# Performance work log

Hardware: AMD Instinct MI355X
Metric: run time of the kernel (lower is better)

## Reference

```python
import jax, jax.numpy as jnp
from jax import lax
import numpy as np

B, D, H, T = 64, 32, 512, 1024


def setup_inputs() -> dict:
    key = jax.random.key(0)
    ks = jax.random.split(key, 7)
    s = 1.0 / np.sqrt(H)
    return {
        "input_data": jax.random.normal(ks[0], (B, D, T), dtype=jnp.float32),
        "W_ih": jax.random.uniform(ks[1], (4 * H, D), jnp.float32, -s, s),
        "W_hh": jax.random.uniform(ks[2], (4 * H, H), jnp.float32, -s, s),
        "b_ih": jax.random.uniform(ks[3], (4 * H,), jnp.float32, -s, s),
        "b_hh": jax.random.uniform(ks[4], (4 * H,), jnp.float32, -s, s),
        "conv_w": jax.random.uniform(ks[5], (1, H, 1), jnp.float32, -s, s),
        "conv_b": jax.random.uniform(ks[6], (1,), jnp.float32, -s, s),
    }


def reference(input_data, W_ih, W_hh, b_ih, b_hh, conv_w, conv_b):
    # (B, D, T) -> (T, B, D), seq-first like torch nn.LSTM
    x = jnp.transpose(input_data, (2, 0, 1))
    # Precompute input-to-gate projections for all timesteps: (T, B, 4H)
    xproj = jnp.einsum('tbd,gd->tbg', x, W_ih) + b_ih + b_hh
    h0 = jnp.zeros((x.shape[1], H), x.dtype)
    c0 = jnp.zeros((x.shape[1], H), x.dtype)

    def step(carry, xp):
        h, c = carry
        gates = xp + h @ W_hh.T  # (B, 4H)
        i, f, g, o = jnp.split(gates, 4, axis=-1)  # torch gate order: i, f, g, o
        i = jax.nn.sigmoid(i)
        f = jax.nn.sigmoid(f)
        g = jnp.tanh(g)
        o = jax.nn.sigmoid(o)
        c_new = f * c + i * g
        h_new = o * jnp.tanh(c_new)
        return (h_new, c_new), h_new

    _, hs = lax.scan(step, (h0, c0), xproj)  # hs: (T, B, H)
    out = jnp.transpose(hs, (1, 2, 0))  # (B, H, T)
    # Conv1d(H, 1, kernel=1) == per-timestep linear
    pred = jnp.einsum('bht,oh->bot', out, conv_w[:, :, 0]) + conv_b[:, None]
    return pred  # (B, 1, T)
```

## Files before the change

### kernel.cpp

```cpp
#include <hip/hip_runtime.h>
#include <hip/hip_bf16.h>


typedef unsigned short ushort_t;
typedef unsigned int   uint_t;
typedef unsigned long long u64_t;
typedef __attribute__((ext_vector_type(8))) short bf16x8;
typedef __attribute__((ext_vector_type(4))) float f32x4;
typedef __attribute__((ext_vector_type(4))) uint_t u32x4;

#define T_STEPS 1024
#define HID     512
#define KDIM    544
#define NBLK    128
#define NTHR    256

__device__ inline ushort_t f2bf(float x) {
    __hip_bfloat16 h = __float2bfloat16(x);
    return *(ushort_t*)&h;
}
__device__ inline float bf2f(ushort_t u) {
    __hip_bfloat16 h = *(__hip_bfloat16*)&u;
    return __bfloat162float(h);
}

__device__ inline f32x4 MFMA(bf16x8 a, bf16x8 b, f32x4 c) {
    return __builtin_amdgcn_mfma_f32_16x16x32_bf16(a, b, c, 0, 0, 0);
}

__device__ inline u32x4 cld16(const void* p) {
    u32x4 v;
    asm volatile("global_load_dwordx4 %0, %1, off sc0 sc1"
                 : "=v"(v) : "v"(p) : "memory");
    return v;
}
__device__ inline void cst4(void* p, uint_t v) {
    asm volatile("global_store_dword %0, %1, off sc0 sc1"
                 :: "v"(p), "v"(v) : "memory");
}
__device__ inline void waitvm0() {
    asm volatile("s_waitcnt vmcnt(0)" ::: "memory");
}

__device__ inline float act_gate(float v, int is_tanh) {
    float vc = fminf(fmaxf(v, -43.f), 43.f);
    float kk = is_tanh ? -2.88539008f : -1.44269504f;
    float e  = __builtin_exp2f(vc * kk);
    float num = is_tanh ? (1.f - e) : 1.f;
    return num * __builtin_amdgcn_rcpf(1.f + e);
}


__global__ void k_init(uint_t* hx32) {
    int i = blockIdx.x * 256 + threadIdx.x;
    hx32[i] = 0x00010000u;
}

__global__ void k_wcat(const float* __restrict__ wih, const float* __restrict__ whh,
                       ushort_t* __restrict__ wh, ushort_t* __restrict__ wl) {
    int r = blockIdx.x;
    for (int k = threadIdx.x; k < KDIM; k += 256) {
        float w = (k < 512) ? whh[r * 512 + k] : wih[r * 32 + (k - 512)];
        ushort_t hh = f2bf(w);
        ushort_t ll = f2bf(w - bf2f(hh));
        wh[r * KDIM + k] = hh;
        wl[r * KDIM + k] = ll;
    }
}

__global__ void k_xbuf(const float* __restrict__ in,
                       ushort_t* __restrict__ xh, ushort_t* __restrict__ xl) {
    __shared__ float tile[64][65];
    int bp = blockIdx.x >> 4;
    int tt = blockIdx.x & 15;
    int t0 = tt * 64;
    int wv = threadIdx.x >> 6, l = threadIdx.x & 63;
    for (int r = wv * 16; r < wv * 16 + 16; r++) {
        int b = bp * 2 + (r >> 5), d = r & 31;
        tile[r][l] = in[(b * 32 + d) * 1024 + t0 + l];
    }
    __syncthreads();
    for (int i = 0; i < 16; i++) {
        int tl = wv * 16 + i;
        float v = tile[l][tl];
        ushort_t hh = f2bf(v);
        ushort_t ll = f2bf(v - bf2f(hh));
        int o = (t0 + tl) * 2048 + bp * 64 + l;
        xh[o] = hh;
        xl[o] = ll;
    }
}

__global__ void k_reduce(const float* __restrict__ part, float* __restrict__ out,
                         const float* __restrict__ cvb) {
    int b = blockIdx.x >> 2;
    int t = (blockIdx.x & 3) * 256 + threadIdx.x;
    int g = b >> 4, bl = b & 15;
    const float* p = part + ((size_t)(g * 32 * 16 + bl)) * 1024 + t;
    float sum = 0.f;
    #pragma unroll
    for (int s = 0; s < 32; s++) sum += p[(size_t)s * 16 * 1024];
    out[b * 1024 + t] = sum + cvb[0];
}


__global__ __launch_bounds__(NTHR, 2) void k_lstm(
    const ushort_t* __restrict__ wh, const ushort_t* __restrict__ wlo,
    const ushort_t* __restrict__ xh, const ushort_t* __restrict__ xl,
    char* hx,
    const float* __restrict__ bih, const float* __restrict__ bhh,
    const float* __restrict__ convw, float* __restrict__ part)
{
    const int tid = threadIdx.x;
    const int w   = tid >> 6;
    const int l   = tid & 63;
    const int g   = blockIdx.x >> 5;
    const int s   = blockIdx.x & 31;
    const int n   = l & 15;
    const int q   = l >> 4;
    const int j   = s * 16 + w * 4 + q;
    const int roww = (n & 3) * HID + s * 16 + w * 4 + (n >> 2);
    const int b0  = g * 16;
    const int wg  = s * 4 + w;

    __shared__ u64_t hs[2][4096];
    __shared__ float projsh[4][16][32];

    bf16x8 Bh[17], Bl[17];
    #pragma unroll
    for (int c = 0; c < 17; c++) {
        Bh[c] = *(const bf16x8*)(wh  + roww * KDIM + c * 32 + q * 8);
        Bl[c] = *(const bf16x8*)(wlo + roww * KDIM + c * 32 + q * 8);
    }

    float bias4[4];
    #pragma unroll
    for (int r = 0; r < 4; r++) bias4[r] = bih[r * HID + j] + bhh[r * HID + j];
    const float cw = convw[j];
    float cst = 0.f;

    const int m16 = tid & 15;
    const int hi4 = tid >> 4;
    const int sq  = (hi4 >> 1) & 3, sd = hi4 & 1, chalf = hi4 >> 3;

    __syncthreads();

    union frag { u64_t d[2]; bf16x8 v; };

    for (int t = 0; t < T_STEPS; t++) {
        frag Ax, Lx;
        {
            int xo = (t * 64 + b0 + n) * 32 + q * 8;
            Ax.v = *(const bf16x8*)(xh + xo);
            Lx.v = *(const bf16x8*)(xl + xo);
        }

        const char* srcB = hx + (size_t)(((t & 1) * 4 + g)) * 32768 + tid * 16;
        u32x4 hv[8];
        #pragma unroll
        for (int k = 0; k < 8; k++) hv[k] = cld16(srcB + k * 4096);
        waitvm0();
        if (t > 0) {
            const uint_t exp = ((uint_t)(((t - 1) >> 1) & 1)) << 16;
            for (;;) {
                bool ok = true;
                #pragma unroll
                for (int k = 0; k < 8; k++) {
                    if (((hv[k][0] & 0x10000u) != exp) ||
                        ((hv[k][1] & 0x10000u) != exp) ||
                        ((hv[k][2] & 0x10000u) != exp) ||
                        ((hv[k][3] & 0x10000u) != exp)) {
                        hv[k] = cld16(srcB + k * 4096);
                        ok = false;
                    }
                }
                if (ok) break;
                __builtin_amdgcn_s_sleep(1);
                waitvm0();
            }
        }
        {
            const int buf = t & 1;
            #pragma unroll
            for (int k = 0; k < 8; k++) {
                uint_t I0 = hv[k][0], I1 = hv[k][1];
                uint_t I2 = hv[k][2], I3 = hv[k][3];
                uint_t hA = __builtin_amdgcn_perm(I1, I0, 0x05040100u);
                uint_t hB = __builtin_amdgcn_perm(I3, I2, 0x05040100u);
                uint_t lA = __builtin_amdgcn_perm(I1, I0, 0x07060302u);
                uint_t lB = __builtin_amdgcn_perm(I3, I2, 0x07060302u);
                int c  = k * 2 + chalf;
                int li = ((c * 4 + sq) * 16 + m16) * 2 + sd;
                hs[buf][li]        = (u64_t)hA | ((u64_t)hB << 32);
                hs[buf][li + 2048] = (u64_t)lA | ((u64_t)lB << 32);
            }
        }
        __syncthreads();

        const int buf = t & 1;
        f32x4 a0 = {0,0,0,0}, a1 = {0,0,0,0}, a2 = {0,0,0,0},
              a3 = {0,0,0,0}, a4 = {0,0,0,0}, a5 = {0,0,0,0};
        #pragma unroll
        for (int c = 0; c < 16; c++) {
            frag Ah, Al;
            int li = ((c * 4 + q) * 16 + n) * 2;
            Ah.v = *(const bf16x8*)&hs[buf][li];
            Al.v = *(const bf16x8*)&hs[buf][li + 2048];
            if (c & 1) {
                a1 = MFMA(Bh[c], Ah.v, a1);
                a3 = MFMA(Bl[c], Ah.v, a3);
                a5 = MFMA(Bh[c], Al.v, a5);
            } else {
                a0 = MFMA(Bh[c], Ah.v, a0);
                a2 = MFMA(Bl[c], Ah.v, a2);
                a4 = MFMA(Bh[c], Al.v, a4);
            }
        }
        {
            a0 = MFMA(Bh[16], Ax.v, a0);
            a2 = MFMA(Bl[16], Ax.v, a2);
            a4 = MFMA(Bh[16], Lx.v, a4);
        }
        f32x4 D = (a0 + a1) + (a2 + a3) + (a4 + a5);

        char* dstB = hx + (size_t)((((t + 1) & 1) * 4 + g) * 128 + wg) * 256;
        const uint_t tag32 = ((uint_t)((t >> 1) & 1)) << 16;
        float iv = act_gate(D[0] + bias4[0], 0);
        float fv = act_gate(D[1] + bias4[1], 0);
        float gv = act_gate(D[2] + bias4[2], 1);
        float ov = act_gate(D[3] + bias4[3], 0);
        float cc = fv * cst + iv * gv;
        cst = cc;
        float th = act_gate(cc, 1);
        float h  = ov * th;
        float pr = cw * h;
        {
            ushort_t hb = f2bf(h);
            uint_t hvp = (uint_t)hb;
            uint_t lvp = (uint_t)f2bf(h - bf2f(hb));
            uint_t word = (hvp | (lvp << 16)) & ~0x10000u;
            word |= tag32;
            cst4(dstB + n * 16 + q * 4, word);
        }

        pr += __shfl_xor(pr, 16);
        pr += __shfl_xor(pr, 32);
        if (l < 16) projsh[w][l][t & 31] = pr;
        if ((t & 31) == 31) {
            __syncthreads();
            int b = tid >> 4, tl0 = tid & 15;
            float* dpt = part + (size_t)((g * 32 + s) * 16 + b) * 1024 + (t - 31);
            #pragma unroll
            for (int hh2 = 0; hh2 < 2; hh2++) {
                int tl = tl0 + hh2 * 16;
                float v = (projsh[0][b][tl] + projsh[1][b][tl]) +
                          (projsh[2][b][tl] + projsh[3][b][tl]);
                __builtin_nontemporal_store(v, dpt + tl);
            }
            __syncthreads();
        }
    }
}

extern "C" void kernel_launch(void* const* d_in, const int* in_sizes, int n_in,
                              void* d_out, int out_size, void* d_ws, size_t ws_size,
                              hipStream_t stream) {
    const float* in  = (const float*)d_in[0];
    const float* Wih = (const float*)d_in[1];
    const float* Whh = (const float*)d_in[2];
    const float* bih = (const float*)d_in[3];
    const float* bhh = (const float*)d_in[4];
    const float* cvw = (const float*)d_in[5];
    const float* cvb = (const float*)d_in[6];
    float* out = (float*)d_out;

    char* ws = (char*)d_ws;
    ushort_t* wh  = (ushort_t*)ws; ws += (size_t)2048 * KDIM * 2;
    ushort_t* wl  = (ushort_t*)ws; ws += (size_t)2048 * KDIM * 2;
    ushort_t* xh  = (ushort_t*)ws; ws += (size_t)1024 * 64 * 32 * 2;
    ushort_t* xl  = (ushort_t*)ws; ws += (size_t)1024 * 64 * 32 * 2;
    char*     hx  = ws;            ws += (size_t)2 * 4 * 128 * 16 * 16;
    float*    pp  = (float*)ws;    ws += (size_t)128 * 16 * 1024 * 4;

    k_init<<<256, 256, 0, stream>>>((uint_t*)hx);
    k_wcat<<<2048, 256, 0, stream>>>(Wih, Whh, wh, wl);
    k_xbuf<<<512, 256, 0, stream>>>(in, xh, xl);
    k_lstm<<<NBLK, NTHR, 0, stream>>>(wh, wl, xh, xl, hx,
                                      bih, bhh, cvw, pp);
    k_reduce<<<256, 256, 0, stream>>>(pp, out, cvb);
}
```

Baseline: 3.131 ms.

## Interleave two batch groups per block to overlap polling with compute

```diff
diff --git a/kernel.cpp b/kernel.cpp
--- a/kernel.cpp
+++ b/kernel.cpp
@@ -12,7 +12,7 @@
 #define T_STEPS 1024
 #define HID     512
 #define KDIM    544
-#define NBLK    128
+#define NBLK    64
 #define NTHR    256
 
 __device__ inline ushort_t f2bf(float x) {
@@ -104,6 +104,95 @@
 }
 
 
+#define STAGE(HS, HV) do {                                              \
+    _Pragma("unroll")                                                   \
+    for (int k_ = 0; k_ < 8; k_++) {                                    \
+        uint_t I0 = HV[k_][0], I1 = HV[k_][1];                          \
+        uint_t I2 = HV[k_][2], I3 = HV[k_][3];                          \
+        uint_t hA_ = __builtin_amdgcn_perm(I1, I0, 0x05040100u);        \
+        uint_t hB_ = __builtin_amdgcn_perm(I3, I2, 0x05040100u);        \
+        uint_t lA_ = __builtin_amdgcn_perm(I1, I0, 0x07060302u);        \
+        uint_t lB_ = __builtin_amdgcn_perm(I3, I2, 0x07060302u);        \
+        int c_  = k_ * 2 + chalf;                                       \
+        int li_ = ((c_ * 4 + sq) * 16 + m16) * 2 + sd;                  \
+        HS[li_]        = (u64_t)hA_ | ((u64_t)hB_ << 32);               \
+        HS[li_ + 2048] = (u64_t)lA_ | ((u64_t)lB_ << 32);               \
+    }                                                                   \
+} while (0)
+
+#define CHECKPOLL(HV, SRC) do {                                         \
+    const uint_t exp_ = ((uint_t)(((t - 1) >> 1) & 1)) << 16;           \
+    for (;;) {                                                          \
+        bool ok_ = true;                                                \
+        _Pragma("unroll")                                               \
+        for (int k_ = 0; k_ < 8; k_++) {                                \
+            if (((HV[k_][0] & 0x10000u) != exp_) ||                     \
+                ((HV[k_][1] & 0x10000u) != exp_) ||                     \
+                ((HV[k_][2] & 0x10000u) != exp_) ||                     \
+                ((HV[k_][3] & 0x10000u) != exp_)) {                     \
+                HV[k_] = cld16((SRC) + k_ * 4096);                      \
+                ok_ = false;                                            \
+            }                                                           \
+        }                                                               \
+        if (ok_) break;                                                 \
+        __builtin_amdgcn_s_sleep(1);                                    \
+        waitvm0();                                                      \
+        __builtin_amdgcn_sched_barrier(0);                              \
+    }                                                                   \
+} while (0)
+
+#define CHUNK(HS, c) do {                                               \
+    frag Ah_, Al_;                                                      \
+    int li_ = (((c) * 4 + q) * 16 + n) * 2;                             \
+    Ah_.v = *(const bf16x8*)&HS[li_];                                   \
+    Al_.v = *(const bf16x8*)&HS[li_ + 2048];                            \
+    if ((c) & 1) {                                                      \
+        a1 = MFMA(Bh[c], Ah_.v, a1);                                    \
+        a3 = MFMA(Bl[c], Ah_.v, a3);                                    \
+        a5 = MFMA(Bh[c], Al_.v, a5);                                    \
+    } else {                                                            \
+        a0 = MFMA(Bh[c], Ah_.v, a0);                                    \
+        a2 = MFMA(Bl[c], Ah_.v, a2);                                    \
+        a4 = MFMA(Bh[c], Al_.v, a4);                                    \
+    }                                                                   \
+} while (0)
+
+#define EPI(Dv, CSTv, GXv, PJv) do {                                    \
+    char* dst_ = hx + (size_t)((((t + 1) & 1) * 4 + (GXv)) * 128 + wg) * 256; \
+    const uint_t tag_ = ((uint_t)((t >> 1) & 1)) << 16;                 \
+    float iv_ = act_gate(Dv[0] + bias4[0], 0);                          \
+    float fv_ = act_gate(Dv[1] + bias4[1], 0);                          \
+    float gv_ = act_gate(Dv[2] + bias4[2], 1);                          \
+    float ov_ = act_gate(Dv[3] + bias4[3], 0);                          \
+    float cc_ = fv_ * (CSTv) + iv_ * gv_;                               \
+    (CSTv) = cc_;                                                       \
+    float h_ = ov_ * act_gate(cc_, 1);                                  \
+    float pr_ = cw * h_;                                                \
+    {                                                                   \
+        ushort_t hb_ = f2bf(h_);                                        \
+        uint_t word_ = (((uint_t)hb_) |                                 \
+                        (((uint_t)f2bf(h_ - bf2f(hb_))) << 16)) & ~0x10000u; \
+        word_ |= tag_;                                                  \
+        cst4(dst_ + n * 16 + q * 4, word_);                             \
+    }                                                                   \
+    pr_ += __shfl_xor(pr_, 16);                                         \
+    pr_ += __shfl_xor(pr_, 32);                                         \
+    if (l < 16) PJv[w][l][t & 31] = pr_;                                \
+    if ((t & 31) == 31) {                                               \
+        __syncthreads();                                                \
+        int b_ = tid >> 4, tl0_ = tid & 15;                             \
+        float* dpt_ = part + (size_t)(((GXv) * 32 + s) * 16 + b_) * 1024 + (t - 31); \
+        _Pragma("unroll")                                               \
+        for (int h2_ = 0; h2_ < 2; h2_++) {                             \
+            int tl_ = tl0_ + h2_ * 16;                                  \
+            float v_ = (PJv[0][b_][tl_] + PJv[1][b_][tl_]) +            \
+                       (PJv[2][b_][tl_] + PJv[3][b_][tl_]);             \
+            __builtin_nontemporal_store(v_, dpt_ + tl_);                \
+        }                                                               \
+        __syncthreads();                                                \
+    }                                                                   \
+} while (0)
+
 __global__ __launch_bounds__(NTHR, 2) void k_lstm(
     const ushort_t* __restrict__ wh, const ushort_t* __restrict__ wlo,
     const ushort_t* __restrict__ xh, const ushort_t* __restrict__ xl,
@@ -114,17 +203,22 @@
     const int tid = threadIdx.x;
     const int w   = tid >> 6;
     const int l   = tid & 63;
-    const int g   = blockIdx.x >> 5;
+    const int gp  = blockIdx.x >> 5;
     const int s   = blockIdx.x & 31;
+    const int gA  = gp * 2;
+    const int gB  = gp * 2 + 1;
     const int n   = l & 15;
     const int q   = l >> 4;
     const int j   = s * 16 + w * 4 + q;
     const int roww = (n & 3) * HID + s * 16 + w * 4 + (n >> 2);
-    const int b0  = g * 16;
+    const int b0A = gA * 16;
+    const int b0B = gB * 16;
     const int wg  = s * 4 + w;
 
-    __shared__ u64_t hs[2][4096];
-    __shared__ float projsh[4][16][32];
+    __shared__ u64_t hsA[4096];
+    __shared__ u64_t hsB[4096];
+    __shared__ float pjA[4][16][32];
+    __shared__ float pjB[4][16][32];
 
     bf16x8 Bh[17], Bl[17];
     #pragma unroll
@@ -137,7 +231,7 @@
     #pragma unroll
     for (int r = 0; r < 4; r++) bias4[r] = bih[r * HID + j] + bhh[r * HID + j];
     const float cw = convw[j];
-    float cst = 0.f;
+    float cstA = 0.f, cstB = 0.f;
 
     const int m16 = tid & 15;
     const int hi4 = tid >> 4;
@@ -145,119 +239,70 @@
 
     __syncthreads();
 
-    union frag { u64_t d[2]; bf16x8 v; };
+    union frag { u32x4 u; bf16x8 v; };
+    u32x4 hvA[8], hvB[8];
+    bf16x8 AxA, LxA, AxB, LxB;
+
+    {
+        const char* sA0 = hx + (size_t)gA * 32768 + tid * 16;
+        #pragma unroll
+        for (int k = 0; k < 8; k++) hvA[k] = cld16(sA0 + k * 4096);
+        int xo = (0 * 64 + b0A + n) * 32 + q * 8;
+        AxA = *(const bf16x8*)(xh + xo);
+        LxA = *(const bf16x8*)(xl + xo);
+    }
 
     for (int t = 0; t < T_STEPS; t++) {
-        frag Ax, Lx;
+        const char* srcCA = hx + (size_t)(((t & 1) * 4 + gA)) * 32768 + tid * 16;
+        waitvm0();
+        __builtin_amdgcn_sched_barrier(0);
+        if (t > 0) CHECKPOLL(hvA, srcCA);
+        STAGE(hsA, hvA);
+        __syncthreads();
         {
-            int xo = (t * 64 + b0 + n) * 32 + q * 8;
-            Ax.v = *(const bf16x8*)(xh + xo);
-            Lx.v = *(const bf16x8*)(xl + xo);
-        }
-
-        const char* srcB = hx + (size_t)(((t & 1) * 4 + g)) * 32768 + tid * 16;
-        u32x4 hv[8];
-        #pragma unroll
-        for (int k = 0; k < 8; k++) hv[k] = cld16(srcB + k * 4096);
-        waitvm0();
-        if (t > 0) {
-            const uint_t exp = ((uint_t)(((t - 1) >> 1) & 1)) << 16;
-            for (;;) {
-                bool ok = true;
-                #pragma unroll
-                for (int k = 0; k < 8; k++) {
-                    if (((hv[k][0] & 0x10000u) != exp) ||
-                        ((hv[k][1] & 0x10000u) != exp) ||
-                        ((hv[k][2] & 0x10000u) != exp) ||
-                        ((hv[k][3] & 0x10000u) != exp)) {
-                        hv[k] = cld16(srcB + k * 4096);
-                        ok = false;
-                    }
-                }
-                if (ok) break;
-                __builtin_amdgcn_s_sleep(1);
-                waitvm0();
-            }
+            const char* sB = hx + (size_t)(((t & 1) * 4 + gB)) * 32768 + tid * 16;
+            #pragma unroll
+            for (int k = 0; k < 8; k++) hvB[k] = cld16(sB + k * 4096);
+            int xo = (t * 64 + b0B + n) * 32 + q * 8;
+            AxB = *(const bf16x8*)(xh + xo);
+            LxB = *(const bf16x8*)(xl + xo);
         }
         {
-            const int buf = t & 1;
+            f32x4 a0 = {0,0,0,0}, a1 = {0,0,0,0}, a2 = {0,0,0,0},
+                  a3 = {0,0,0,0}, a4 = {0,0,0,0}, a5 = {0,0,0,0};
             #pragma unroll
-            for (int k = 0; k < 8; k++) {
-                uint_t I0 = hv[k][0], I1 = hv[k][1];
-                uint_t I2 = hv[k][2], I3 = hv[k][3];
-                uint_t hA = __builtin_amdgcn_perm(I1, I0, 0x05040100u);
-                uint_t hB = __builtin_amdgcn_perm(I3, I2, 0x05040100u);
-                uint_t lA = __builtin_amdgcn_perm(I1, I0, 0x07060302u);
-                uint_t lB = __builtin_amdgcn_perm(I3, I2, 0x07060302u);
-                int c  = k * 2 + chalf;
-                int li = ((c * 4 + sq) * 16 + m16) * 2 + sd;
-                hs[buf][li]        = (u64_t)hA | ((u64_t)hB << 32);
-                hs[buf][li + 2048] = (u64_t)lA | ((u64_t)lB << 32);
-            }
+            for (int c = 0; c < 16; c++) CHUNK(hsA, c);
+            a0 = MFMA(Bh[16], AxA, a0);
+            a2 = MFMA(Bl[16], AxA, a2);
+            a4 = MFMA(Bh[16], LxA, a4);
+            f32x4 D = (a0 + a1) + (a2 + a3) + (a4 + a5);
+            EPI(D, cstA, gA, pjA);
         }
+
+        const char* srcCB = hx + (size_t)(((t & 1) * 4 + gB)) * 32768 + tid * 16;
+        waitvm0();
+        __builtin_amdgcn_sched_barrier(0);
+        if (t > 0) CHECKPOLL(hvB, srcCB);
+        STAGE(hsB, hvB);
         __syncthreads();
-
-        const int buf = t & 1;
-        f32x4 a0 = {0,0,0,0}, a1 = {0,0,0,0}, a2 = {0,0,0,0},
-              a3 = {0,0,0,0}, a4 = {0,0,0,0}, a5 = {0,0,0,0};
-        #pragma unroll
-        for (int c = 0; c < 16; c++) {
-            frag Ah, Al;
-            int li = ((c * 4 + q) * 16 + n) * 2;
-            Ah.v = *(const bf16x8*)&hs[buf][li];
-            Al.v = *(const bf16x8*)&hs[buf][li + 2048];
-            if (c & 1) {
-                a1 = MFMA(Bh[c], Ah.v, a1);
-                a3 = MFMA(Bl[c], Ah.v, a3);
-                a5 = MFMA(Bh[c], Al.v, a5);
-            } else {
-                a0 = MFMA(Bh[c], Ah.v, a0);
-                a2 = MFMA(Bl[c], Ah.v, a2);
-                a4 = MFMA(Bh[c], Al.v, a4);
-            }
+        if (t + 1 < T_STEPS) {
+            const char* sAn = hx + (size_t)((((t + 1) & 1) * 4 + gA)) * 32768 + tid * 16;
+            #pragma unroll
+            for (int k = 0; k < 8; k++) hvA[k] = cld16(sAn + k * 4096);
+            int xo = ((t + 1) * 64 + b0A + n) * 32 + q * 8;
+            AxA = *(const bf16x8*)(xh + xo);
+            LxA = *(const bf16x8*)(xl + xo);
         }
         {
-            a0 = MFMA(Bh[16], Ax.v, a0);
-            a2 = MFMA(Bl[16], Ax.v, a2);
-            a4 = MFMA(Bh[16], Lx.v, a4);
-        }
-        f32x4 D = (a0 + a1) + (a2 + a3) + (a4 + a5);
-
-        char* dstB = hx + (size_t)((((t + 1) & 1) * 4 + g) * 128 + wg) * 256;
-        const uint_t tag32 = ((uint_t)((t >> 1) & 1)) << 16;
-        float iv = act_gate(D[0] + bias4[0], 0);
-        float fv = act_gate(D[1] + bias4[1], 0);
-        float gv = act_gate(D[2] + bias4[2], 1);
-        float ov = act_gate(D[3] + bias4[3], 0);
-        float cc = fv * cst + iv * gv;
-        cst = cc;
-        float th = act_gate(cc, 1);
-        float h  = ov * th;
-        float pr = cw * h;
-        {
-            ushort_t hb = f2bf(h);
-            uint_t hvp = (uint_t)hb;
-            uint_t lvp = (uint_t)f2bf(h - bf2f(hb));
-            uint_t word = (hvp | (lvp << 16)) & ~0x10000u;
-            word |= tag32;
-            cst4(dstB + n * 16 + q * 4, word);
-        }
-
-        pr += __shfl_xor(pr, 16);
-        pr += __shfl_xor(pr, 32);
-        if (l < 16) projsh[w][l][t & 31] = pr;
-        if ((t & 31) == 31) {
-            __syncthreads();
-            int b = tid >> 4, tl0 = tid & 15;
-            float* dpt = part + (size_t)((g * 32 + s) * 16 + b) * 1024 + (t - 31);
+            f32x4 a0 = {0,0,0,0}, a1 = {0,0,0,0}, a2 = {0,0,0,0},
+                  a3 = {0,0,0,0}, a4 = {0,0,0,0}, a5 = {0,0,0,0};
             #pragma unroll
-            for (int hh2 = 0; hh2 < 2; hh2++) {
-                int tl = tl0 + hh2 * 16;
-                float v = (projsh[0][b][tl] + projsh[1][b][tl]) +
-                          (projsh[2][b][tl] + projsh[3][b][tl]);
-                __builtin_nontemporal_store(v, dpt + tl);
-            }
-            __syncthreads();
+            for (int c = 0; c < 16; c++) CHUNK(hsB, c);
+            a0 = MFMA(Bh[16], AxB, a0);
+            a2 = MFMA(Bl[16], AxB, a2);
+            a4 = MFMA(Bh[16], LxB, a4);
+            f32x4 D = (a0 + a1) + (a2 + a3) + (a4 + a5);
+            EPI(D, cstB, gB, pjB);
         }
     }
 }
```

New measurement: 7.675 ms. 2.45x slower.
